# Optimization experiments

Hardware: AMD Instinct MI355X
Metric: run time of the kernel (lower is better)

The kernel has to match this reference:

```python
import jax, jax.numpy as jnp
import numpy as np

B, K, H, W, N = 256, 16, 64, 64, 1024   # batch, channels (n_ch), grid H/W, sampled sites
F_IN = 9 * K - 1                         # 3x3 neighborhood * K channels, minus center channel


def setup_inputs() -> dict:
    key = jax.random.key(0)
    ks = jax.random.split(key, 8)
    z_int = jax.random.randint(ks[0], (B, K, H, W), 0, 16, dtype=jnp.int32)
    bs = jax.random.randint(ks[1], (N,), 0, K, dtype=jnp.int32)
    ii = jax.random.randint(ks[2], (N,), 0, H, dtype=jnp.int32)
    jj = jax.random.randint(ks[3], (N,), 0, W, dtype=jnp.int32)
    W1 = jax.random.normal(ks[4], (F_IN, 128), dtype=jnp.float32) * 0.05
    b1 = jnp.zeros((128,), dtype=jnp.float32)
    W2 = jax.random.normal(ks[5], (128, 16), dtype=jnp.float32) * 0.05
    b2 = jnp.zeros((16,), dtype=jnp.float32)
    return {"z_int": z_int, "bs": bs, "ii": ii, "jj": jj,
            "W1": W1, "b1": b1, "W2": W2, "b2": b2}


def _gather_ctx(z_f, bs, ii, jj):
    # Faithful to get_context ordering: loops di, dj (each in [-1,0,1]) then b,
    # skipping (di==0, dj==0, b==bi). Flattened skip position = 4*K + bi.
    off = jnp.array([-1, 0, 1], dtype=jnp.int32)
    di = jnp.repeat(off, 3)          # [9]
    dj = jnp.tile(off, 3)            # [9]
    ni = (ii[:, None] + di[None, :]) % H   # [N, 9] toroidal wrap
    nj = (jj[:, None] + dj[None, :]) % W   # [N, 9]
    ctx = z_f[:, :, ni, nj]                # [B, K, N, 9]
    ctx = jnp.transpose(ctx, (2, 0, 3, 1)).reshape(N, B, 9 * K)  # [N, B, 9K], (di,dj) major then b
    drop = 4 * K + bs                      # [N] center-channel flat index
    idx = jnp.arange(F_IN, dtype=jnp.int32)
    keep = idx[None, :] + (idx[None, :] >= drop[:, None]).astype(jnp.int32)  # [N, F_IN]
    return jax.vmap(lambda c, k: c[:, k])(ctx, keep)  # [N, B, F_IN]


def reference(z_int, bs, ii, jj, W1, b1, W2, b2):
    z_f = z_int.astype(jnp.float32) / 15.0
    ctx = _gather_ctx(z_f, bs, ii, jj)                 # [N, B, 9K-1]
    h = jax.nn.relu(jnp.einsum('nbf,fh->nbh', ctx, W1) + b1)
    logits = jnp.einsum('nbh,hc->nbc', h, W2) + b2     # [N, B, 16]
    pred = jnp.argmax(logits, axis=-1)                 # [N, B]
    tgt = z_int[:, bs, ii, jj].T                       # [N, B]
    rate = jnp.mean((pred != tgt).astype(jnp.float32)) # np.mean of per-site mean == global mean
    return rate
```

## Files before the change

### kernel.cpp

```cpp
#include <hip/hip_runtime.h>
#include <stdint.h>

#define NB 1024
#define BB 256
#define KK 16
#define HH 64
#define WW 64
#define F_FULL 144
#define HDIM 128
#define CDIM 16
#define KPAD 160
#define APITCH 160
#define HPITCH 136
#define ABYTES (64 * APITCH * 2)
#define NCTR 128

typedef __bf16 bf16x8 __attribute__((ext_vector_type(8)));
typedef float f32x4 __attribute__((ext_vector_type(4)));

#define W1T_OFF 1024
#define W1T_BYTES (16 * HDIM * KPAD * 2)
#define W2B_OFF (W1T_OFF + W1T_BYTES)
#define W2B_BYTES (CDIM * HDIM * 2)
#define ZT_OFF (W2B_OFF + W2B_BYTES)

__device__ __forceinline__ unsigned short bf16_bits(float v) {
    __bf16 b = (__bf16)v;
    return __builtin_bit_cast(unsigned short, b);
}

__device__ __forceinline__ int a_off(int row, int gran) {
    return row * APITCH + (((gran & ~7) | ((gran & 7) ^ (row & 7))) << 3);
}

#define TP 144
__global__ __launch_bounds__(256) void prep_kernel(
    const int* __restrict__ z, const float* __restrict__ W1,
    const float* __restrict__ W2, uint8_t* __restrict__ zt,
    unsigned short* __restrict__ W1t, unsigned short* __restrict__ W2b,
    int* __restrict__ counters) {
    int bid = blockIdx.x;
    int t = threadIdx.x;
    if (bid < 4096) {
        __shared__ uint8_t tile[32 * TP];
        int bx = bid & 127;
        int by = bid >> 7;
        int c0 = bx * 32, r0 = by * 128;
#pragma unroll
        for (int i = 0; i < 4; ++i) {
            int lin = i * 256 + t;
            int c = lin & 31;
            int rq = lin >> 5;
            uchar4 v;
            v.x = (uint8_t)z[(size_t)(r0 + rq * 4 + 0) * 4096 + c0 + c];
            v.y = (uint8_t)z[(size_t)(r0 + rq * 4 + 1) * 4096 + c0 + c];
            v.z = (uint8_t)z[(size_t)(r0 + rq * 4 + 2) * 4096 + c0 + c];
            v.w = (uint8_t)z[(size_t)(r0 + rq * 4 + 3) * 4096 + c0 + c];
            *(uchar4*)(tile + c * TP + rq * 4) = v;
        }
        __syncthreads();
        int cy = t >> 3, rx = t & 7;
        uint4 v = *(const uint4*)(tile + cy * TP + rx * 16);
        *(uint4*)(zt + (size_t)(c0 + cy) * 4096 + r0 + rx * 16) = v;
    } else if (bid < 5376) {
        int idx = (bid - 4096) * 256 + t;
        int k = idx % KPAD;
        int h = (idx / KPAD) % HDIM;
        int s = idx / (KPAD * HDIM);
        int drop = 4 * KK + s;
        float val = 0.0f;
        if (k < F_FULL && k != drop) {
            int src = k - (k > drop ? 1 : 0);
            val = W1[src * HDIM + h];
        }
        W1t[idx] = bf16_bits(val);
    } else {
        int idx = (bid - 5376) * 256 + t;
        if (idx < CDIM * HDIM) {
            int k = idx % HDIM;
            int c = idx / HDIM;
            W2b[idx] = bf16_bits(W2[k * CDIM + c]);
        }
        if (bid == 5376 && t < NCTR) counters[t] = 0;
    }
}

__global__ __launch_bounds__(256, 4) void main_kernel(
    const uint8_t* __restrict__ zt, const unsigned short* __restrict__ W1t,
    const float* __restrict__ b1, const unsigned short* __restrict__ W2b,
    const float* __restrict__ b2, const int* __restrict__ bs,
    const int* __restrict__ ii, const int* __restrict__ jj,
    int* __restrict__ counters) {
    __shared__ __align__(16) unsigned char smem[2 * ABYTES];
    unsigned short* sA0 = (unsigned short*)smem;
    unsigned short* sA1 = (unsigned short*)(smem + ABYTES);

    int t = threadIdx.x;
    int n = blockIdx.x;
    int wave = t >> 6, lane = t & 63;
    int l15 = lane & 15, l4 = lane >> 4;

    int in_ = ii[n], jn = jj[n], sn = bs[n];

    const unsigned short* w1s = W1t + (size_t)sn * (HDIM * KPAD);
    int n0 = wave * 32;
    bf16x8 Bf[2][5];
#pragma unroll
    for (int nt = 0; nt < 2; ++nt)
#pragma unroll
        for (int ks = 0; ks < 5; ++ks)
            Bf[nt][ks] = *(const bf16x8*)(w1s + (n0 + nt * 16 + l15) * KPAD + ks * 32 + l4 * 8);
    bf16x8 Bf2[4];
#pragma unroll
    for (int ks = 0; ks < 4; ++ks)
        Bf2[ks] = *(const bf16x8*)(W2b + l15 * HDIM + ks * 32 + l4 * 8);
    float b1v0 = b1[n0 + l15], b1v1 = b1[n0 + 16 + l15];
    float b2v = b2[l15];

    {
        int b = t & 63, gran = 18 + ((t >> 6) & 1);
        unsigned short* dstp = (t >= 128) ? sA1 : sA0;
        *(uint4*)(dstp + a_off(b, gran)) = make_uint4(0, 0, 0, 0);
    }

    uint4 g0, g1, g2;
    auto gload = [&](int tile) {
        int b = (t & 63) + tile * 64;
        int p0 = t >> 6;
        int ni0 = (in_ + p0 / 3 - 1) & (HH - 1);
        int nj0 = (jn + p0 % 3 - 1) & (WW - 1);
        g0 = *(const uint4*)(zt + (((size_t)(ni0 * WW + nj0) * BB + b) << 4));
        int p1 = p0 + 4;
        int ni1 = (in_ + p1 / 3 - 1) & (HH - 1);
        int nj1 = (jn + p1 % 3 - 1) & (WW - 1);
        g1 = *(const uint4*)(zt + (((size_t)(ni1 * WW + nj1) * BB + b) << 4));
        if (t < 64) {
            int ni2 = (in_ + 1) & (HH - 1);
            int nj2 = (jn + 1) & (WW - 1);
            g2 = *(const uint4*)(zt + (((size_t)(ni2 * WW + nj2) * BB + b) << 4));
        }
    };
    auto gwrite = [&](unsigned short* dst) {
        int b = t & 63;
        int p0 = t >> 6;
        auto conv = [&](uint4 raw, int p) {
            const uint8_t* bytes = (const uint8_t*)&raw;
            union { __bf16 h[16]; uint4 q[2]; } u;
#pragma unroll
            for (int k = 0; k < 16; ++k)
                u.h[k] = (__bf16)((float)bytes[k] * (1.0f / 15.0f));
            *(uint4*)(dst + a_off(b, 2 * p)) = u.q[0];
            *(uint4*)(dst + a_off(b, 2 * p + 1)) = u.q[1];
        };
        conv(g0, p0);
        conv(g1, p0 + 4);
        if (t < 64) conv(g2, 8);
    };

    gload(0);
    gwrite(sA0);
    int err = 0;
    size_t tbase = ((size_t)(in_ * WW + jn) * BB) << 4;

    for (int tile = 0; tile < 4; ++tile) {
        unsigned short* sA = (tile & 1) ? sA1 : sA0;
        unsigned short* sH = sA;
        unsigned short* sAnext = (tile & 1) ? sA0 : sA1;

        if (tile < 3) gload(tile + 1);
        __syncthreads();

        f32x4 acc[4][2] = {};
#pragma unroll
        for (int mt = 0; mt < 4; ++mt) {
            bf16x8 Af[5];
#pragma unroll
            for (int ks = 0; ks < 5; ++ks)
                Af[ks] = *(const bf16x8*)(sA + a_off(mt * 16 + l15, 4 * ks + l4 * 0 + l4));
#pragma unroll
            for (int ks = 0; ks < 5; ++ks) {
                acc[mt][0] = __builtin_amdgcn_mfma_f32_16x16x32_bf16(Af[ks], Bf[0][ks], acc[mt][0], 0, 0, 0);
                acc[mt][1] = __builtin_amdgcn_mfma_f32_16x16x32_bf16(Af[ks], Bf[1][ks], acc[mt][1], 0, 0, 0);
            }
        }
        __syncthreads();

#pragma unroll
        for (int mt = 0; mt < 4; ++mt)
#pragma unroll
            for (int nt = 0; nt < 2; ++nt) {
                float bv = nt ? b1v1 : b1v0;
                int hcol = n0 + nt * 16 + l15;
#pragma unroll
                for (int r = 0; r < 4; ++r) {
                    int b = mt * 16 + l4 * 4 + r;
                    float v = fmaxf(acc[mt][nt][r] + bv, 0.0f);
                    sH[b * HPITCH + hcol] = bf16_bits(v);
                }
            }
        __syncthreads();

        f32x4 acc2 = {};
#pragma unroll
        for (int ks = 0; ks < 4; ++ks) {
            bf16x8 Af = *(const bf16x8*)(sH + (wave * 16 + l15) * HPITCH + ks * 32 + l4 * 8);
            acc2 = __builtin_amdgcn_mfma_f32_16x16x32_bf16(Af, Bf2[ks], acc2, 0, 0, 0);
        }

#pragma unroll
        for (int r = 0; r < 4; ++r) {
            float v = acc2[r] + b2v;
            int idx = l15;
#pragma unroll
            for (int m = 1; m < 16; m <<= 1) {
                float ov = __shfl_xor(v, m);
                int oi = __shfl_xor(idx, m);
                if (ov > v || (ov == v && oi < idx)) { v = ov; idx = oi; }
            }
            int bg = tile * 64 + wave * 16 + l4 * 4 + r;
            int tgt = zt[tbase + ((size_t)bg << 4) + sn];
            unsigned long long mm = __ballot(l15 == 0 && idx != tgt);
            err += (int)__popcll(mm);
        }

        if (tile < 3) gwrite(sAnext);
    }

    if (lane == 0) atomicAdd(&counters[n & (NCTR - 1)], err);
}

__global__ void finalize_kernel(const int* __restrict__ counters, float* __restrict__ out) {
    int t = threadIdx.x;
    int s = counters[t] + counters[t + 64];
#pragma unroll
    for (int m = 32; m; m >>= 1) s += __shfl_down(s, m);
    if (t == 0) out[0] = (float)s / (float)(NB * BB);
}

extern "C" void kernel_launch(void* const* d_in, const int* in_sizes, int n_in,
                              void* d_out, int out_size, void* d_ws, size_t ws_size,
                              hipStream_t stream) {
    const int* z = (const int*)d_in[0];
    const int* bs = (const int*)d_in[1];
    const int* ii = (const int*)d_in[2];
    const int* jj = (const int*)d_in[3];
    const float* W1 = (const float*)d_in[4];
    const float* b1 = (const float*)d_in[5];
    const float* W2 = (const float*)d_in[6];
    const float* b2 = (const float*)d_in[7];
    float* out = (float*)d_out;

    uint8_t* ws = (uint8_t*)d_ws;
    int* counters = (int*)ws;
    unsigned short* W1t = (unsigned short*)(ws + W1T_OFF);
    unsigned short* W2b = (unsigned short*)(ws + W2B_OFF);
    uint8_t* zt = ws + ZT_OFF;

    prep_kernel<<<5384, 256, 0, stream>>>(z, W1, W2, zt, W1t, W2b, counters);
    main_kernel<<<NB, 256, 0, stream>>>(zt, W1t, b1, W2b, b2, bs, ii, jj, counters);
    finalize_kernel<<<1, 64, 0, stream>>>(counters, out);
}
```

Baseline: 153.7 us.

## Pre-convert grid to bf16 and stage context tiles via direct global-to-LDS loads

The prep kernel now writes the transposed grid as bf16 values already divided by 15, so the main kernel no longer converts uint8 to bf16 per tile. Context tiles are copied straight into a plain (unswizzled) LDS layout with global_load_lds, replacing the register-staged load/convert/write double buffer. The target class is recovered from the bf16 value, and W2 fragments are reloaded per k-step instead of being held in registers. This cuts VALU work and register pressure, but doubles the bytes of the transposed grid written and read, and the unswizzled LDS layout may cause bank conflicts.

Measured after the change: 144.6 us. 1.06x faster.

```diff
diff --git a/kernel.cpp b/kernel.cpp
--- a/kernel.cpp
+++ b/kernel.cpp
@@ -10,9 +10,9 @@
 #define HDIM 128
 #define CDIM 16
 #define KPAD 160
-#define APITCH 160
 #define HPITCH 136
-#define ABYTES (64 * APITCH * 2)
+#define PBYTES 2048
+#define ABYTES (10 * PBYTES)
 #define NCTR 128
 
 typedef __bf16 bf16x8 __attribute__((ext_vector_type(8)));
@@ -22,21 +22,17 @@
 #define W1T_BYTES (16 * HDIM * KPAD * 2)
 #define W2B_OFF (W1T_OFF + W1T_BYTES)
 #define W2B_BYTES (CDIM * HDIM * 2)
-#define ZT_OFF (W2B_OFF + W2B_BYTES)
+#define ZTB_OFF (W2B_OFF + W2B_BYTES)
 
 __device__ __forceinline__ unsigned short bf16_bits(float v) {
     __bf16 b = (__bf16)v;
     return __builtin_bit_cast(unsigned short, b);
 }
 
-__device__ __forceinline__ int a_off(int row, int gran) {
-    return row * APITCH + (((gran & ~7) | ((gran & 7) ^ (row & 7))) << 3);
-}
-
 #define TP 144
 __global__ __launch_bounds__(256) void prep_kernel(
     const int* __restrict__ z, const float* __restrict__ W1,
-    const float* __restrict__ W2, uint8_t* __restrict__ zt,
+    const float* __restrict__ W2, uint8_t* __restrict__ ztb,
     unsigned short* __restrict__ W1t, unsigned short* __restrict__ W2b,
     int* __restrict__ counters) {
     int bid = blockIdx.x;
@@ -61,7 +57,14 @@
         __syncthreads();
         int cy = t >> 3, rx = t & 7;
         uint4 v = *(const uint4*)(tile + cy * TP + rx * 16);
-        *(uint4*)(zt + (size_t)(c0 + cy) * 4096 + r0 + rx * 16) = v;
+        const uint8_t* bytes = (const uint8_t*)&v;
+        union { __bf16 h[16]; uint4 q[2]; } u;
+#pragma unroll
+        for (int k = 0; k < 16; ++k)
+            u.h[k] = (__bf16)((float)bytes[k] * (1.0f / 15.0f));
+        uint4* dst = (uint4*)(ztb + (((size_t)(c0 + cy) * 4096 + r0 + rx * 16) << 1));
+        dst[0] = u.q[0];
+        dst[1] = u.q[1];
     } else if (bid < 5376) {
         int idx = (bid - 4096) * 256 + t;
         int k = idx % KPAD;
@@ -86,14 +89,12 @@
 }
 
 __global__ __launch_bounds__(256, 4) void main_kernel(
-    const uint8_t* __restrict__ zt, const unsigned short* __restrict__ W1t,
+    const uint8_t* __restrict__ ztb, const unsigned short* __restrict__ W1t,
     const float* __restrict__ b1, const unsigned short* __restrict__ W2b,
     const float* __restrict__ b2, const int* __restrict__ bs,
     const int* __restrict__ ii, const int* __restrict__ jj,
     int* __restrict__ counters) {
     __shared__ __align__(16) unsigned char smem[2 * ABYTES];
-    unsigned short* sA0 = (unsigned short*)smem;
-    unsigned short* sA1 = (unsigned short*)(smem + ABYTES);
 
     int t = threadIdx.x;
     int n = blockIdx.x;
@@ -102,6 +103,28 @@
 
     int in_ = ii[n], jn = jj[n], sn = bs[n];
 
+    auto stage = [&](int buf, int tile) {
+#pragma unroll
+        for (int j = 0; j < 5; ++j) {
+            int it = wave + j * 4;
+            if (it < 18) {
+                int p = it >> 1, half = it & 1;
+                int di = (p * 11) >> 5;
+                int dj = p - di * 3;
+                int ni = (in_ + di - 1) & (HH - 1);
+                int nj = (jn + dj - 1) & (WW - 1);
+                const uint8_t* src = ztb + ((size_t)(ni * WW + nj) << 13)
+                                   + ((tile * 64 + half * 32) << 5) + lane * 16;
+                __builtin_amdgcn_global_load_lds(
+                    (const __attribute__((address_space(1))) void*)src,
+                    (__attribute__((address_space(3))) void*)(smem + buf * ABYTES + p * PBYTES + half * 1024),
+                    16, 0, 0);
+            }
+        }
+    };
+
+    stage(0, 0);
+
     const unsigned short* w1s = W1t + (size_t)sn * (HDIM * KPAD);
     int n0 = wave * 32;
     bf16x8 Bf[2][5];
@@ -110,65 +133,28 @@
 #pragma unroll
         for (int ks = 0; ks < 5; ++ks)
             Bf[nt][ks] = *(const bf16x8*)(w1s + (n0 + nt * 16 + l15) * KPAD + ks * 32 + l4 * 8);
-    bf16x8 Bf2[4];
-#pragma unroll
-    for (int ks = 0; ks < 4; ++ks)
-        Bf2[ks] = *(const bf16x8*)(W2b + l15 * HDIM + ks * 32 + l4 * 8);
     float b1v0 = b1[n0 + l15], b1v1 = b1[n0 + 16 + l15];
     float b2v = b2[l15];
 
     {
-        int b = t & 63, gran = 18 + ((t >> 6) & 1);
-        unsigned short* dstp = (t >= 128) ? sA1 : sA0;
-        *(uint4*)(dstp + a_off(b, gran)) = make_uint4(0, 0, 0, 0);
+        int buf = t >> 7;
+        *(uint4*)(smem + buf * ABYTES + 9 * PBYTES + (t & 127) * 16) = make_uint4(0, 0, 0, 0);
     }
 
-    uint4 g0, g1, g2;
-    auto gload = [&](int tile) {
-        int b = (t & 63) + tile * 64;
-        int p0 = t >> 6;
-        int ni0 = (in_ + p0 / 3 - 1) & (HH - 1);
-        int nj0 = (jn + p0 % 3 - 1) & (WW - 1);
-        g0 = *(const uint4*)(zt + (((size_t)(ni0 * WW + nj0) * BB + b) << 4));
-        int p1 = p0 + 4;
-        int ni1 = (in_ + p1 / 3 - 1) & (HH - 1);
-        int nj1 = (jn + p1 % 3 - 1) & (WW - 1);
-        g1 = *(const uint4*)(zt + (((size_t)(ni1 * WW + nj1) * BB + b) << 4));
-        if (t < 64) {
-            int ni2 = (in_ + 1) & (HH - 1);
-            int nj2 = (jn + 1) & (WW - 1);
-            g2 = *(const uint4*)(zt + (((size_t)(ni2 * WW + nj2) * BB + b) << 4));
-        }
-    };
-    auto gwrite = [&](unsigned short* dst) {
-        int b = t & 63;
-        int p0 = t >> 6;
-        auto conv = [&](uint4 raw, int p) {
-            const uint8_t* bytes = (const uint8_t*)&raw;
-            union { __bf16 h[16]; uint4 q[2]; } u;
-#pragma unroll
-            for (int k = 0; k < 16; ++k)
-                u.h[k] = (__bf16)((float)bytes[k] * (1.0f / 15.0f));
-            *(uint4*)(dst + a_off(b, 2 * p)) = u.q[0];
-            *(uint4*)(dst + a_off(b, 2 * p + 1)) = u.q[1];
-        };
-        conv(g0, p0);
-        conv(g1, p0 + 4);
-        if (t < 64) conv(g2, 8);
-    };
-
-    gload(0);
-    gwrite(sA0);
-    int err = 0;
-    size_t tbase = ((size_t)(in_ * WW + jn) * BB) << 4;
+    int err = 0, cur = 0;
+    size_t tb8 = ((size_t)(in_ * WW + jn) << 13);
 
     for (int tile = 0; tile < 4; ++tile) {
-        unsigned short* sA = (tile & 1) ? sA1 : sA0;
-        unsigned short* sH = sA;
-        unsigned short* sAnext = (tile & 1) ? sA0 : sA1;
-
-        if (tile < 3) gload(tile + 1);
-        __syncthreads();
+        __syncthreads();
+        if (tile < 3) stage(cur ^ 1, tile + 1);
+
+        int bg0 = tile * 64 + wave * 16 + l4 * 4;
+        unsigned short tv[4];
+#pragma unroll
+        for (int r = 0; r < 4; ++r)
+            tv[r] = *(const unsigned short*)(ztb + tb8 + ((size_t)(bg0 + r) << 5) + (sn << 1));
+
+        const unsigned short* sAs = (const unsigned short*)(smem + cur * ABYTES);
 
         f32x4 acc[4][2] = {};
 #pragma unroll
@@ -176,7 +162,7 @@
             bf16x8 Af[5];
 #pragma unroll
             for (int ks = 0; ks < 5; ++ks)
-                Af[ks] = *(const bf16x8*)(sA + a_off(mt * 16 + l15, 4 * ks + l4 * 0 + l4));
+                Af[ks] = *(const bf16x8*)(sAs + (2 * ks + (l4 >> 1)) * 1024 + (mt * 16 + l15) * 16 + (l4 & 1) * 8);
 #pragma unroll
             for (int ks = 0; ks < 5; ++ks) {
                 acc[mt][0] = __builtin_amdgcn_mfma_f32_16x16x32_bf16(Af[ks], Bf[0][ks], acc[mt][0], 0, 0, 0);
@@ -185,6 +171,7 @@
         }
         __syncthreads();
 
+        unsigned short* sH = (unsigned short*)(smem + cur * ABYTES);
 #pragma unroll
         for (int mt = 0; mt < 4; ++mt)
 #pragma unroll
@@ -203,8 +190,9 @@
         f32x4 acc2 = {};
 #pragma unroll
         for (int ks = 0; ks < 4; ++ks) {
+            bf16x8 Bf2 = *(const bf16x8*)(W2b + l15 * HDIM + ks * 32 + l4 * 8);
             bf16x8 Af = *(const bf16x8*)(sH + (wave * 16 + l15) * HPITCH + ks * 32 + l4 * 8);
-            acc2 = __builtin_amdgcn_mfma_f32_16x16x32_bf16(Af, Bf2[ks], acc2, 0, 0, 0);
+            acc2 = __builtin_amdgcn_mfma_f32_16x16x32_bf16(Af, Bf2, acc2, 0, 0, 0);
         }
 
 #pragma unroll
@@ -217,13 +205,13 @@
                 int oi = __shfl_xor(idx, m);
                 if (ov > v || (ov == v && oi < idx)) { v = ov; idx = oi; }
             }
-            int bg = tile * 64 + wave * 16 + l4 * 4 + r;
-            int tgt = zt[tbase + ((size_t)bg << 4) + sn];
+            float tf = __builtin_bit_cast(float, (uint32_t)tv[r] << 16);
+            int tgt = (int)(tf * 15.0f + 0.5f);
             unsigned long long mm = __ballot(l15 == 0 && idx != tgt);
             err += (int)__popcll(mm);
         }
 
-        if (tile < 3) gwrite(sAnext);
+        cur ^= 1;
     }
 
     if (lane == 0) atomicAdd(&counters[n & (NCTR - 1)], err);
@@ -254,9 +242,9 @@
     int* counters = (int*)ws;
     unsigned short* W1t = (unsigned short*)(ws + W1T_OFF);
     unsigned short* W2b = (unsigned short*)(ws + W2B_OFF);
-    uint8_t* zt = ws + ZT_OFF;
-
-    prep_kernel<<<5384, 256, 0, stream>>>(z, W1, W2, zt, W1t, W2b, counters);
-    main_kernel<<<NB, 256, 0, stream>>>(zt, W1t, b1, W2b, b2, bs, ii, jj, counters);
+    uint8_t* ztb = ws + ZTB_OFF;
+
+    prep_kernel<<<5384, 256, 0, stream>>>(z, W1, W2, ztb, W1t, W2b, counters);
+    main_kernel<<<NB, 256, 0, stream>>>(ztb, W1t, b1, W2b, b2, bs, ii, jj, counters);
     finalize_kernel<<<1, 64, 0, stream>>>(counters, out);
 }
```
